# Kernel tuning notes

Measured on AMD Instinct MI355X. Metric: run time of the kernel, lower is better.

The kernel has to match this reference:

```python
import jax, jax.numpy as jnp
import numpy as np

N = 50000
E = 800000
HID = 128
OUT = 64
HEADS = 4
NEG_SLOPE = 0.2


def gat_layer(x, edge_index, W, att_src, att_dst, bias):
    """PyG-style GATConv: shared linear for src/dst, additive attention,
    self-loops, segment softmax over incoming edges, concat heads + bias."""
    n = x.shape[0]
    H, C = att_src.shape
    # add self loops (PyG default add_self_loops=True)
    loops = jnp.arange(n, dtype=edge_index.dtype)
    src = jnp.concatenate([edge_index[0], loops])  # message sources j
    dst = jnp.concatenate([edge_index[1], loops])  # aggregation targets i
    xl = (x @ W).reshape(n, H, C)                  # [N,H,C]
    a_s = jnp.einsum('nhc,hc->nh', xl, att_src)    # [N,H]
    a_d = jnp.einsum('nhc,hc->nh', xl, att_dst)    # [N,H]
    e = jax.nn.leaky_relu(a_s[src] + a_d[dst], NEG_SLOPE)   # [E',H]
    m = jax.ops.segment_max(e, dst, num_segments=n)         # stable softmax
    e = jnp.exp(e - m[dst])
    denom = jax.ops.segment_sum(e, dst, num_segments=n)
    alpha = e / (denom[dst] + 1e-16)                        # [E',H]
    msg = xl[src] * alpha[:, :, None]                       # [E',H,C]
    out = jax.ops.segment_sum(msg, dst, num_segments=n)     # [N,H,C]
    return out.reshape(n, H * C) + bias


def setup_inputs() -> dict:
    key = jax.random.key(0)
    ks = jax.random.split(key, 16)
    C = HID // HEADS  # per-head channels = 32
    x = jax.random.normal(ks[0], (N, HID), dtype=jnp.float32)
    edge_indices = jax.random.randint(ks[1], (3, 2, E), 0, N, dtype=jnp.int32)
    s = 0.1
    inp = {
        'x': x,
        'edge_indices': edge_indices,
        'W1': jax.random.normal(ks[2], (HID, HEADS * C), dtype=jnp.float32) * s,
        'as1': jax.random.normal(ks[3], (HEADS, C), dtype=jnp.float32) * s,
        'ad1': jax.random.normal(ks[4], (HEADS, C), dtype=jnp.float32) * s,
        'b1': jnp.zeros((HEADS * C,), dtype=jnp.float32),
        'W2': jax.random.normal(ks[5], (HID, HEADS * C), dtype=jnp.float32) * s,
        'as2': jax.random.normal(ks[6], (HEADS, C), dtype=jnp.float32) * s,
        'ad2': jax.random.normal(ks[7], (HEADS, C), dtype=jnp.float32) * s,
        'b2': jnp.zeros((HEADS * C,), dtype=jnp.float32),
        'W3': jax.random.normal(ks[8], (HID, OUT), dtype=jnp.float32) * s,
        'as3': jax.random.normal(ks[9], (1, OUT), dtype=jnp.float32) * s,
        'ad3': jax.random.normal(ks[10], (1, OUT), dtype=jnp.float32) * s,
        'b3': jnp.zeros((OUT,), dtype=jnp.float32),
    }
    return inp


def reference(x, edge_indices, W1, as1, ad1, b1, W2, as2, ad2, b2, W3, as3, ad3, b3):
    h = jax.nn.relu(gat_layer(x, edge_indices[0], W1, as1, ad1, b1))
    h = jax.nn.relu(gat_layer(h, edge_indices[1], W2, as2, ad2, b2))
    out = gat_layer(h, edge_indices[2], W3, as3, ad3, b3)  # no ReLU on last layer
    return out
```

## Files before the change

kernel.cpp:

```cpp
#include <hip/hip_runtime.h>

typedef unsigned short u16;
typedef unsigned int u32;
typedef __attribute__((ext_vector_type(8))) short short8;
typedef __attribute__((ext_vector_type(4))) float f32x4;

#define HID 128

static inline int cdiv(long long a, int b) { return (int)((a + b - 1) / b); }

__device__ __forceinline__ float bfbits(u32 u) { union { u32 u; float f; } c; c.u = u; return c.f; }
__device__ __forceinline__ u16 f2bf(float f) {
  union { float f; u32 u; } c; c.f = f;
  u32 u = c.u;
  return (u16)((u + 0x7fffu + ((u >> 16) & 1u)) >> 16);
}
__device__ __forceinline__ u32 pack2bf(float a, float b) {
  return (u32)f2bf(a) | ((u32)f2bf(b) << 16);
}

__global__ __launch_bounds__(256) void prep_wt3(
    const float* __restrict__ W1, const float* __restrict__ W2,
    const float* __restrict__ W3, u16* __restrict__ wt1, u16* __restrict__ wt2,
    u16* __restrict__ wt3) {
  int y = blockIdx.y;
  const float* W = (y == 0) ? W1 : ((y == 1) ? W2 : W3);
  u16* WT = (y == 0) ? wt1 : ((y == 1) ? wt2 : wt3);
  int cout = (y == 2) ? 64 : 128;
  int idx = blockIdx.x * 256 + threadIdx.x;
  if (idx < 128 * cout) {
    int k = idx / cout, c = idx - k * cout;
    WT[c * 128 + k] = f2bf(W[idx]);
  }
}

template <int COUT, int HEADS, bool BF16IN>
__global__ __launch_bounds__(256) void gemm_attn_mfma(
    const void* __restrict__ HinV, const u16* __restrict__ WT,
    const float* __restrict__ attS, const float* __restrict__ attD,
    u16* __restrict__ XL, float* __restrict__ aS, float* __restrict__ aD, int n) {
  constexpr int NT = COUT / 16;
  constexpr int C = COUT / HEADS;
  constexpr int TPH = C / 16;

  int t = threadIdx.x;
  int wv = t >> 6, ln = t & 63;
  int lrow = ln & 15;
  int lk = ln >> 4;
  int row = blockIdx.x * 64 + wv * 16 + lrow;
  bool ok = (row < n);
  int rowc = ok ? row : (n - 1);

  short8 bb[4];
  if (BF16IN) {
    const u16* hp = (const u16*)HinV + (size_t)rowc * HID;
#pragma unroll
    for (int kb = 0; kb < 4; ++kb)
      bb[kb] = *(const short8*)(hp + kb * 32 + lk * 8);
  } else {
    const float* hp = (const float*)HinV + (size_t)rowc * HID;
    float4 hv[8];
#pragma unroll
    for (int kb = 0; kb < 4; ++kb) {
      hv[2 * kb] = *(const float4*)(hp + kb * 32 + lk * 8);
      hv[2 * kb + 1] = *(const float4*)(hp + kb * 32 + lk * 8 + 4);
    }
#pragma unroll
    for (int kb = 0; kb < 4; ++kb) {
      union { short8 s; u32 u[4]; } pk;
      float4 h0 = hv[2 * kb], h1 = hv[2 * kb + 1];
      pk.u[0] = pack2bf(h0.x, h0.y);
      pk.u[1] = pack2bf(h0.z, h0.w);
      pk.u[2] = pack2bf(h1.x, h1.y);
      pk.u[3] = pack2bf(h1.z, h1.w);
      bb[kb] = pk.s;
    }
  }

  f32x4 acc[NT];
#pragma unroll
  for (int ct = 0; ct < NT; ++ct) acc[ct] = {0.f, 0.f, 0.f, 0.f};

#pragma unroll
  for (int kb = 0; kb < 4; ++kb) {
    const u16* wp = WT + (size_t)lrow * HID + kb * 32 + lk * 8;
#pragma unroll
    for (int ct = 0; ct < NT; ++ct) {
      short8 aw = *(const short8*)(wp + (size_t)ct * 16 * HID);
      acc[ct] = __builtin_amdgcn_mfma_f32_16x16x32_bf16(aw, bb[kb], acc[ct], 0, 0, 0);
    }
  }

  float pS[HEADS], pD[HEADS];
#pragma unroll
  for (int h = 0; h < HEADS; ++h) { pS[h] = 0.f; pD[h] = 0.f; }
#pragma unroll
  for (int ct = 0; ct < NT; ++ct) {
    float4 sv = *(const float4*)(attS + ct * 16 + lk * 4);
    float4 dv = *(const float4*)(attD + ct * 16 + lk * 4);
    int h = ct / TPH;
    pS[h] += acc[ct][0] * sv.x + acc[ct][1] * sv.y + acc[ct][2] * sv.z + acc[ct][3] * sv.w;
    pD[h] += acc[ct][0] * dv.x + acc[ct][1] * dv.y + acc[ct][2] * dv.z + acc[ct][3] * dv.w;
  }
#pragma unroll
  for (int h = 0; h < HEADS; ++h) {
    pS[h] += __shfl_xor(pS[h], 16);
    pS[h] += __shfl_xor(pS[h], 32);
    pD[h] += __shfl_xor(pD[h], 16);
    pD[h] += __shfl_xor(pD[h], 32);
  }
  if (lk == 0 && ok) {
    if (HEADS == 4) {
      *(float4*)(aS + (size_t)row * 4) = make_float4(pS[0], pS[1], pS[2], pS[3]);
      *(float4*)(aD + (size_t)row * 4) = make_float4(pD[0], pD[1], pD[2], pD[3]);
    } else {
      aS[row] = pS[0];
      aD[row] = pD[0];
    }
  }

  if (ok) {
    u32* Xp = (u32*)XL + (size_t)row * (COUT / 2);
#pragma unroll
    for (int ct = 0; ct < NT; ++ct) {
      *(uint2*)(Xp + ct * 8 + lk * 2) =
          make_uint2(pack2bf(acc[ct][0], acc[ct][1]), pack2bf(acc[ct][2], acc[ct][3]));
    }
  }
}

#define PSTR 16

__global__ __launch_bounds__(256) void bucket_hist(const int* __restrict__ ei,
                                                   int* __restrict__ cntP,
                                                   int e4, int rem, int E, int NB) {
  int L = blockIdx.y;
  const int* dst = ei + (size_t)(2 * L + 1) * E;
  __shared__ int cnt[256];
  int t = threadIdx.x;
  cnt[t] = 0;
  __syncthreads();
  int gbase = blockIdx.x * 1024 + t;
#pragma unroll
  for (int u = 0; u < 4; ++u) {
    int g = gbase + u * 256;
    if (g < e4) {
      int4 d = *(const int4*)(dst + g * 4);
      atomicAdd(&cnt[d.x >> 8], 1);
      atomicAdd(&cnt[d.y >> 8], 1);
      atomicAdd(&cnt[d.z >> 8], 1);
      atomicAdd(&cnt[d.w >> 8], 1);
    }
  }
  if (blockIdx.x == 0 && t < rem) atomicAdd(&cnt[dst[e4 * 4 + t] >> 8], 1);
  __syncthreads();
  int c = cnt[t];
  if (t < NB && c > 0) atomicAdd(&cntP[(L * NB + t) * PSTR], c);
}

__global__ __launch_bounds__(256) void bucket_scan(const int* __restrict__ cntP,
                                                   int* __restrict__ bucketOff,
                                                   int* __restrict__ curP, int NB, int E) {
  int L = blockIdx.x;
  int t = threadIdx.x;
  int lane = t & 63, wid = t >> 6;
  __shared__ int wpart[4];
  int v = (t < NB) ? cntP[(L * NB + t) * PSTR] : 0;
  int inc = v;
#pragma unroll
  for (int off = 1; off < 64; off <<= 1) {
    int w = __shfl_up(inc, (unsigned)off, 64);
    if (lane >= off) inc += w;
  }
  if (lane == 63) wpart[wid] = inc;
  __syncthreads();
  if (t == 0) {
    int a = 0;
#pragma unroll
    for (int k = 0; k < 4; ++k) { int tmp = wpart[k]; wpart[k] = a; a += tmp; }
  }
  __syncthreads();
  int ex = wpart[wid] + inc - v;
  if (t < NB) {
    bucketOff[L * (NB + 1) + t] = ex;
    curP[(L * NB + t) * PSTR] = ex;
  }
  if (t == 0) bucketOff[L * (NB + 1) + NB] = E;
}

__global__ __launch_bounds__(256) void bucket_scatter(const int* __restrict__ ei,
                                                      int* __restrict__ curP,
                                                      u32* __restrict__ pairsAll,
                                                      int e4, int rem, int E, int NB) {
  int L = blockIdx.y;
  const int* src = ei + (size_t)(2 * L) * E;
  const int* dst = src + E;
  u32* pairs = pairsAll + (size_t)L * E;
  __shared__ int cnt[256];
  __shared__ int baseS[256];
  int t = threadIdx.x;
  cnt[t] = 0;
  __syncthreads();

  int gbase = blockIdx.x * 1024 + t;
  int4 dv[4], sv[4];
  bool val[4];
#pragma unroll
  for (int u = 0; u < 4; ++u) {
    int g = gbase + u * 256;
    val[u] = (g < e4);
    if (val[u]) {
      dv[u] = *(const int4*)(dst + g * 4);
      sv[u] = *(const int4*)(src + g * 4);
      atomicAdd(&cnt[dv[u].x >> 8], 1);
      atomicAdd(&cnt[dv[u].y >> 8], 1);
      atomicAdd(&cnt[dv[u].z >> 8], 1);
      atomicAdd(&cnt[dv[u].w >> 8], 1);
    }
  }
  int tailS = 0, tailD = 0;
  bool hasTail = (blockIdx.x == 0 && t < rem);
  if (hasTail) {
    tailD = dst[e4 * 4 + t];
    tailS = src[e4 * 4 + t];
    atomicAdd(&cnt[tailD >> 8], 1);
  }
  __syncthreads();
  int c = cnt[t];
  if (t < NB && c > 0) baseS[t] = atomicAdd(&curP[(L * NB + t) * PSTR], c);
  __syncthreads();
  cnt[t] = 0;
  __syncthreads();
#pragma unroll
  for (int u = 0; u < 4; ++u) {
    if (val[u]) {
      int b, p;
      b = dv[u].x >> 8; p = atomicAdd(&cnt[b], 1);
      pairs[baseS[b] + p] = ((u32)(dv[u].x & 0xff) << 24) | (u32)sv[u].x;
      b = dv[u].y >> 8; p = atomicAdd(&cnt[b], 1);
      pairs[baseS[b] + p] = ((u32)(dv[u].y & 0xff) << 24) | (u32)sv[u].y;
      b = dv[u].z >> 8; p = atomicAdd(&cnt[b], 1);
      pairs[baseS[b] + p] = ((u32)(dv[u].z & 0xff) << 24) | (u32)sv[u].z;
      b = dv[u].w >> 8; p = atomicAdd(&cnt[b], 1);
      pairs[baseS[b] + p] = ((u32)(dv[u].w & 0xff) << 24) | (u32)sv[u].w;
    }
  }
  if (hasTail) {
    int b = tailD >> 8;
    int p = atomicAdd(&cnt[b], 1);
    pairs[baseS[b] + p] = ((u32)(tailD & 0xff) << 24) | (u32)tailS;
  }
}

__global__ __launch_bounds__(256) void csr_finalize(const u32* __restrict__ pairsAll,
                                                    const int* __restrict__ bucketOff,
                                                    int* __restrict__ indptrAll,
                                                    int* __restrict__ srcIdxAll,
                                                    int* __restrict__ dstIdxAll,
                                                    int N, int E, int NB) {
  int L = blockIdx.y, b = blockIdx.x;
  const u32* pairs = pairsAll + (size_t)L * E;
  int* indptr = indptrAll + (size_t)L * (N + 1);
  int* srcL = srcIdxAll + (size_t)L * (E + N);
  int* dstL = dstIdxAll + (size_t)L * (E + N);
  int base = b << 8;
  int nodes = min(256, N - base);
  int p0 = bucketOff[L * (NB + 1) + b];
  int p1 = bucketOff[L * (NB + 1) + b + 1];

  __shared__ int cnt[256];
  __shared__ int wpart[4];
  int t = threadIdx.x;
  int lane = t & 63, wid = t >> 6;
  cnt[t] = 0;
  __syncthreads();

  for (int i = p0 + t; i < p1; i += 256) atomicAdd(&cnt[pairs[i] >> 24], 1);
  __syncthreads();

  int v = (t < nodes) ? cnt[t] + 1 : 0;
  int inc = v;
#pragma unroll
  for (int off = 1; off < 64; off <<= 1) {
    int w = __shfl_up(inc, (unsigned)off, 64);
    if (lane >= off) inc += w;
  }
  if (lane == 63) wpart[wid] = inc;
  __syncthreads();
  if (t == 0) {
    int a = 0;
#pragma unroll
    for (int k = 0; k < 4; ++k) { int tmp = wpart[k]; wpart[k] = a; a += tmp; }
  }
  __syncthreads();
  int ex = wpart[wid] + inc - v;
  __syncthreads();
  if (t < nodes) {
    int segStart = p0 + base + ex;
    indptr[base + t] = segStart;
    srcL[segStart] = base + t;
    dstL[segStart] = base + t;
    cnt[t] = segStart + 1;
  }
  if (b == NB - 1 && t == 0) indptr[N] = E + N;
  __syncthreads();

  for (int i = p0 + t; i < p1; i += 256) {
    u32 pk = pairs[i];
    int d = (int)(pk >> 24);
    int p = atomicAdd(&cnt[d], 1);
    srcL[p] = (int)(pk & 0xffffffu);
    dstL[p] = base + d;
  }
}

template <int HEADS>
__global__ __launch_bounds__(256) void edge_w_ep(
    const float* __restrict__ aS, const float* __restrict__ aD,
    const int* __restrict__ srcL, const int* __restrict__ dstL,
    float* __restrict__ wOut, int ne, int wstride) {
  int e = blockIdx.x * 256 + threadIdx.x;
  if (e >= ne) return;
  int j = srcL[e];
  int i = dstL[e];
  if (HEADS == 4) {
    float4 s4 = *(const float4*)(aS + (size_t)j * 4);
    float4 d4 = *(const float4*)(aD + (size_t)i * 4);
    float l0 = s4.x + d4.x, l1 = s4.y + d4.y, l2 = s4.z + d4.z, l3 = s4.w + d4.w;
    l0 = (l0 >= 0.f) ? l0 : 0.2f * l0;
    l1 = (l1 >= 0.f) ? l1 : 0.2f * l1;
    l2 = (l2 >= 0.f) ? l2 : 0.2f * l2;
    l3 = (l3 >= 0.f) ? l3 : 0.2f * l3;
    wOut[e] = __expf(fminf(l0, 60.f));
    wOut[(size_t)wstride + e] = __expf(fminf(l1, 60.f));
    wOut[(size_t)2 * wstride + e] = __expf(fminf(l2, 60.f));
    wOut[(size_t)3 * wstride + e] = __expf(fminf(l3, 60.f));
  } else {
    float l = aS[j] + aD[i];
    l = (l >= 0.f) ? l : 0.2f * l;
    wOut[e] = __expf(fminf(l, 60.f));
  }
}

template <int COUT, int HEADS, bool RELU, bool OUTBF>
__global__ __launch_bounds__(256, 8) void aggregate(
    const u16* __restrict__ XL, const float* __restrict__ wAll,
    const int* __restrict__ indptr, const int* __restrict__ srcIdx,
    const float* __restrict__ bias, void* __restrict__ outV, int n, int wstride) {
  constexpr int LPN = COUT / 8;
  constexpr int NPW = 64 / LPN;
  constexpr int C = COUT / HEADS;

  int wid = (blockIdx.x * blockDim.x + threadIdx.x) >> 6;
  int lane = threadIdx.x & 63;
  int sub = lane / LPN;
  int cl = lane % LPN;
  int i = wid * NPW + sub;
  bool ok = (i < n);
  int ic = ok ? i : (n - 1);

  int col0 = cl * 8;
  int h = col0 / C;
  int e0 = indptr[ic];
  int deg = indptr[ic + 1] - e0;
  const float* wh = wAll + (size_t)h * wstride;
  const u32* XL32 = (const u32*)XL;

  float s = 0.f;
  float acc[8];
#pragma unroll
  for (int v = 0; v < 8; ++v) acc[v] = 0.f;

  auto cons = [&](float el, const uint4& q) {
    s += el;
    acc[0] += el * bfbits(q.x << 16);
    acc[1] += el * bfbits(q.x & 0xffff0000u);
    acc[2] += el * bfbits(q.y << 16);
    acc[3] += el * bfbits(q.y & 0xffff0000u);
    acc[4] += el * bfbits(q.z << 16);
    acc[5] += el * bfbits(q.z & 0xffff0000u);
    acc[6] += el * bfbits(q.w << 16);
    acc[7] += el * bfbits(q.w & 0xffff0000u);
  };
  auto xlrow = [&](int j) {
    return *(const uint4*)(XL32 + (size_t)j * (COUT / 2) + cl * 4);
  };

  int nbF = deg >> 2;
  int r = deg & 3;

  int4 jA;
  float4 wA;
  if (nbF > 0) {
    jA = *(const int4*)(srcIdx + e0);
    wA = *(const float4*)(wh + e0);
  }
  for (int b = 0; b < nbF; ++b) {
    int4 jC = jA;
    float4 wC = wA;
    if (b + 1 < nbF) {
      jA = *(const int4*)(srcIdx + e0 + (b + 1) * 4);
      wA = *(const float4*)(wh + e0 + (b + 1) * 4);
    }
    uint4 q0 = xlrow(jC.x);
    uint4 q1 = xlrow(jC.y);
    uint4 q2 = xlrow(jC.z);
    uint4 q3 = xlrow(jC.w);
    cons(wC.x, q0);
    cons(wC.y, q1);
    cons(wC.z, q2);
    cons(wC.w, q3);
  }
  if (r) {
    int e = e0 + nbF * 4;
    int j0 = srcIdx[e];
    int j1 = (r > 1) ? srcIdx[e + 1] : 0;
    int j2 = (r > 2) ? srcIdx[e + 2] : 0;
    float w0 = wh[e];
    float w1 = (r > 1) ? wh[e + 1] : 0.f;
    float w2 = (r > 2) ? wh[e + 2] : 0.f;
    uint4 q0 = xlrow(j0);
    uint4 q1 = xlrow(j1);
    uint4 q2 = xlrow(j2);
    cons(w0, q0);
    if (r > 1) cons(w1, q1);
    if (r > 2) cons(w2, q2);
  }

  if (!ok) return;
  float inv = 1.f / (s + 1e-16f);
  float o[8];
#pragma unroll
  for (int v = 0; v < 8; ++v) {
    o[v] = acc[v] * inv + bias[col0 + v];
    if (RELU) o[v] = fmaxf(o[v], 0.f);
  }
  if (OUTBF) {
    u32* op = (u32*)outV + (size_t)i * (COUT / 2) + cl * 4;
    *(uint4*)op = make_uint4(pack2bf(o[0], o[1]), pack2bf(o[2], o[3]),
                             pack2bf(o[4], o[5]), pack2bf(o[6], o[7]));
  } else {
    float* op = (float*)outV + (size_t)i * COUT + col0;
    *(float4*)op = make_float4(o[0], o[1], o[2], o[3]);
    *(float4*)(op + 4) = make_float4(o[4], o[5], o[6], o[7]);
  }
}

extern "C" void kernel_launch(void* const* d_in, const int* in_sizes, int n_in,
                              void* d_out, int out_size, void* d_ws, size_t ws_size,
                              hipStream_t stream) {
  const float* x = (const float*)d_in[0];
  const int* ei = (const int*)d_in[1];
  const float* W1 = (const float*)d_in[2];
  const float* as1 = (const float*)d_in[3];
  const float* ad1 = (const float*)d_in[4];
  const float* b1 = (const float*)d_in[5];
  const float* W2 = (const float*)d_in[6];
  const float* as2 = (const float*)d_in[7];
  const float* ad2 = (const float*)d_in[8];
  const float* b2 = (const float*)d_in[9];
  const float* W3 = (const float*)d_in[10];
  const float* as3 = (const float*)d_in[11];
  const float* ad3 = (const float*)d_in[12];
  const float* b3 = (const float*)d_in[13];

  int N = in_sizes[0] / HID;
  int E = in_sizes[1] / 6;
  int NB = cdiv(N, 256);
  int EN = E + N;

  char* w = (char*)d_ws;
  auto alloc = [&](size_t bytes) {
    void* q = (void*)w;
    w += (bytes + 255) & ~(size_t)255;
    return q;
  };
  u16* bufH = (u16*)alloc((size_t)N * HID * 2);
  u16* bufXL = (u16*)alloc((size_t)N * HID * 2);
  float* aS = (float*)alloc((size_t)N * 4 * 4);
  float* aD = (float*)alloc((size_t)N * 4 * 4);
  float* wEdge = (float*)alloc((size_t)4 * EN * 4);
  u16* wt1 = (u16*)alloc((size_t)128 * 128 * 2);
  u16* wt2 = (u16*)alloc((size_t)128 * 128 * 2);
  u16* wt3 = (u16*)alloc((size_t)64 * 128 * 2);
  int* cntP = (int*)alloc((size_t)3 * NB * PSTR * 4);
  int* curP = (int*)alloc((size_t)3 * NB * PSTR * 4);
  int* bucketOff = (int*)alloc((size_t)3 * (NB + 1) * 4);
  u32* pairsAll = (u32*)alloc((size_t)3 * E * 4);
  int* indptrAll = (int*)alloc((size_t)3 * (N + 1) * 4);
  int* srcIdxAll = (int*)alloc((size_t)3 * EN * 4);
  int* dstIdxAll = (int*)alloc((size_t)3 * EN * 4);

  int e4 = E >> 2, rem = E & 3;
  int gx = cdiv(e4, 1024);
  int gne = cdiv(EN, 256);

  {
    dim3 g(64, 3);
    prep_wt3<<<g, 256, 0, stream>>>(W1, W2, W3, wt1, wt2, wt3);
  }
  hipMemsetAsync(cntP, 0, (size_t)3 * NB * PSTR * 4, stream);
  {
    dim3 g(gx, 3);
    bucket_hist<<<g, 256, 0, stream>>>(ei, cntP, e4, rem, E, NB);
  }
  bucket_scan<<<3, 256, 0, stream>>>(cntP, bucketOff, curP, NB, E);
  {
    dim3 g(gx, 3);
    bucket_scatter<<<g, 256, 0, stream>>>(ei, curP, pairsAll, e4, rem, E, NB);
  }
  {
    dim3 g(NB, 3);
    csr_finalize<<<g, 256, 0, stream>>>(pairsAll, bucketOff, indptrAll, srcIdxAll,
                                        dstIdxAll, N, E, NB);
  }

  gemm_attn_mfma<128, 4, false><<<cdiv(N, 64), 256, 0, stream>>>(
      x, wt1, as1, ad1, bufXL, aS, aD, N);
  edge_w_ep<4><<<gne, 256, 0, stream>>>(aS, aD, srcIdxAll, dstIdxAll, wEdge, EN, EN);
  aggregate<128, 4, true, true><<<cdiv(N, 16), 256, 0, stream>>>(
      bufXL, wEdge, indptrAll, srcIdxAll, b1, bufH, N, EN);
  gemm_attn_mfma<128, 4, true><<<cdiv(N, 64), 256, 0, stream>>>(
      bufH, wt2, as2, ad2, bufXL, aS, aD, N);
  edge_w_ep<4><<<gne, 256, 0, stream>>>(aS, aD, srcIdxAll + (size_t)EN,
                                        dstIdxAll + (size_t)EN, wEdge, EN, EN);
  aggregate<128, 4, true, true><<<cdiv(N, 16), 256, 0, stream>>>(
      bufXL, wEdge, indptrAll + (N + 1), srcIdxAll + (size_t)EN, b2, bufH, N, EN);
  gemm_attn_mfma<64, 1, true><<<cdiv(N, 64), 256, 0, stream>>>(
      bufH, wt3, as3, ad3, bufXL, aS, aD, N);
  edge_w_ep<1><<<gne, 256, 0, stream>>>(aS, aD, srcIdxAll + (size_t)2 * EN,
                                        dstIdxAll + (size_t)2 * EN, wEdge, EN, EN);
  aggregate<64, 1, false, false><<<cdiv(N, 32), 256, 0, stream>>>(
      bufXL, wEdge, indptrAll + 2 * (N + 1), srcIdxAll + (size_t)2 * EN, b3,
      d_out, N, EN);
}
```

Measured before the change: 361.1 us.

## Fold weight prep and layer-1 GEMM into CSR build kernels; stage finalize in LDS

Weight transpose/convert runs as an extra grid row inside the bucket histogram kernel. The layer-1 projection GEMM runs as an extra grid row inside the bucket scatter kernel, so it overlaps with CSR construction and two launches disappear. csr_finalize now builds each bucket's segment in shared memory and writes it out contiguously, falling back to direct global writes when the bucket is too large. The 64 KB of LDS per block can lower finalize occupancy, and the fused kernels mix unrelated work, which may change their register pressure.

```diff
diff --git a/kernel.cpp b/kernel.cpp
--- a/kernel.cpp
+++ b/kernel.cpp
@@ -19,35 +19,19 @@
   return (u32)f2bf(a) | ((u32)f2bf(b) << 16);
 }
 
-__global__ __launch_bounds__(256) void prep_wt3(
-    const float* __restrict__ W1, const float* __restrict__ W2,
-    const float* __restrict__ W3, u16* __restrict__ wt1, u16* __restrict__ wt2,
-    u16* __restrict__ wt3) {
-  int y = blockIdx.y;
-  const float* W = (y == 0) ? W1 : ((y == 1) ? W2 : W3);
-  u16* WT = (y == 0) ? wt1 : ((y == 1) ? wt2 : wt3);
-  int cout = (y == 2) ? 64 : 128;
-  int idx = blockIdx.x * 256 + threadIdx.x;
-  if (idx < 128 * cout) {
-    int k = idx / cout, c = idx - k * cout;
-    WT[c * 128 + k] = f2bf(W[idx]);
-  }
-}
-
 template <int COUT, int HEADS, bool BF16IN>
-__global__ __launch_bounds__(256) void gemm_attn_mfma(
-    const void* __restrict__ HinV, const u16* __restrict__ WT,
+__device__ __forceinline__ void gemm_body(
+    int bx, int t, const void* __restrict__ HinV, const u16* __restrict__ WT,
     const float* __restrict__ attS, const float* __restrict__ attD,
     u16* __restrict__ XL, float* __restrict__ aS, float* __restrict__ aD, int n) {
   constexpr int NT = COUT / 16;
   constexpr int C = COUT / HEADS;
   constexpr int TPH = C / 16;
 
-  int t = threadIdx.x;
   int wv = t >> 6, ln = t & 63;
   int lrow = ln & 15;
   int lk = ln >> 4;
-  int row = blockIdx.x * 64 + wv * 16 + lrow;
+  int row = bx * 64 + wv * 16 + lrow;
   bool ok = (row < n);
   int rowc = ok ? row : (n - 1);
 
@@ -129,11 +113,37 @@
   }
 }
 
+template <int COUT, int HEADS, bool BF16IN>
+__global__ __launch_bounds__(256) void gemm_attn_mfma(
+    const void* __restrict__ HinV, const u16* __restrict__ WT,
+    const float* __restrict__ attS, const float* __restrict__ attD,
+    u16* __restrict__ XL, float* __restrict__ aS, float* __restrict__ aD, int n) {
+  gemm_body<COUT, HEADS, BF16IN>(blockIdx.x, threadIdx.x, HinV, WT, attS, attD,
+                                 XL, aS, aD, n);
+}
+
 #define PSTR 16
 
-__global__ __launch_bounds__(256) void bucket_hist(const int* __restrict__ ei,
-                                                   int* __restrict__ cntP,
-                                                   int e4, int rem, int E, int NB) {
+__global__ __launch_bounds__(256) void bucket_hist_prep(
+    const int* __restrict__ ei, int* __restrict__ cntP, int e4, int rem, int E, int NB,
+    const float* __restrict__ W1, const float* __restrict__ W2,
+    const float* __restrict__ W3, u16* __restrict__ wt1, u16* __restrict__ wt2,
+    u16* __restrict__ wt3) {
+  if (blockIdx.y == 3) {
+    int bx = blockIdx.x;
+    if (bx >= 160) return;
+    int y = (bx >= 128) ? 2 : (bx >= 64 ? 1 : 0);
+    int b0 = (y == 0) ? 0 : ((y == 1) ? 64 : 128);
+    const float* W = (y == 0) ? W1 : ((y == 1) ? W2 : W3);
+    u16* WT = (y == 0) ? wt1 : ((y == 1) ? wt2 : wt3);
+    int cout = (y == 2) ? 64 : 128;
+    int idx = (bx - b0) * 256 + threadIdx.x;
+    if (idx < 128 * cout) {
+      int k = idx / cout, c = idx - k * cout;
+      WT[c * 128 + k] = f2bf(W[idx]);
+    }
+    return;
+  }
   int L = blockIdx.y;
   const int* dst = ei + (size_t)(2 * L + 1) * E;
   __shared__ int cnt[256];
@@ -188,10 +198,18 @@
   if (t == 0) bucketOff[L * (NB + 1) + NB] = E;
 }
 
-__global__ __launch_bounds__(256) void bucket_scatter(const int* __restrict__ ei,
-                                                      int* __restrict__ curP,
-                                                      u32* __restrict__ pairsAll,
-                                                      int e4, int rem, int E, int NB) {
+__global__ __launch_bounds__(256) void bucket_scatter_gemm(
+    const int* __restrict__ ei, int* __restrict__ curP, u32* __restrict__ pairsAll,
+    int e4, int rem, int E, int NB,
+    const float* __restrict__ x, const u16* __restrict__ wt1,
+    const float* __restrict__ as1, const float* __restrict__ ad1,
+    u16* __restrict__ XL, float* __restrict__ aS, float* __restrict__ aD,
+    int n, int ngb) {
+  if (blockIdx.y == 3) {
+    if ((int)blockIdx.x < ngb)
+      gemm_body<128, 4, false>(blockIdx.x, threadIdx.x, x, wt1, as1, ad1, XL, aS, aD, n);
+    return;
+  }
   int L = blockIdx.y;
   const int* src = ei + (size_t)(2 * L) * E;
   const int* dst = src + E;
@@ -252,6 +270,7 @@
   }
 }
 
+#define FCAP 8192
 __global__ __launch_bounds__(256) void csr_finalize(const u32* __restrict__ pairsAll,
                                                     const int* __restrict__ bucketOff,
                                                     int* __restrict__ indptrAll,
@@ -270,6 +289,8 @@
 
   __shared__ int cnt[256];
   __shared__ int wpart[4];
+  __shared__ int sSrc[FCAP];
+  __shared__ int sDst[FCAP];
   int t = threadIdx.x;
   int lane = t & 63, wid = t >> 6;
   cnt[t] = 0;
@@ -294,23 +315,45 @@
   }
   __syncthreads();
   int ex = wpart[wid] + inc - v;
+  int tot = (p1 - p0) + nodes;
+  bool useLds = (tot <= FCAP);
+  int g0 = p0 + base;
   __syncthreads();
   if (t < nodes) {
-    int segStart = p0 + base + ex;
-    indptr[base + t] = segStart;
-    srcL[segStart] = base + t;
-    dstL[segStart] = base + t;
-    cnt[t] = segStart + 1;
+    indptr[base + t] = g0 + ex;
+    if (useLds) {
+      sSrc[ex] = base + t;
+      sDst[ex] = base + t;
+    } else {
+      srcL[g0 + ex] = base + t;
+      dstL[g0 + ex] = base + t;
+    }
+    cnt[t] = ex + 1;
   }
   if (b == NB - 1 && t == 0) indptr[N] = E + N;
   __syncthreads();
 
-  for (int i = p0 + t; i < p1; i += 256) {
-    u32 pk = pairs[i];
-    int d = (int)(pk >> 24);
-    int p = atomicAdd(&cnt[d], 1);
-    srcL[p] = (int)(pk & 0xffffffu);
-    dstL[p] = base + d;
+  if (useLds) {
+    for (int i = p0 + t; i < p1; i += 256) {
+      u32 pk = pairs[i];
+      int d = (int)(pk >> 24);
+      int p = atomicAdd(&cnt[d], 1);
+      sSrc[p] = (int)(pk & 0xffffffu);
+      sDst[p] = base + d;
+    }
+    __syncthreads();
+    for (int k = t; k < tot; k += 256) {
+      srcL[g0 + k] = sSrc[k];
+      dstL[g0 + k] = sDst[k];
+    }
+  } else {
+    for (int i = p0 + t; i < p1; i += 256) {
+      u32 pk = pairs[i];
+      int d = (int)(pk >> 24);
+      int p = atomicAdd(&cnt[d], 1);
+      srcL[g0 + p] = (int)(pk & 0xffffffu);
+      dstL[g0 + p] = base + d;
+    }
   }
 }
 
@@ -493,21 +536,22 @@
 
   int e4 = E >> 2, rem = E & 3;
   int gx = cdiv(e4, 1024);
+  int ngb = cdiv(N, 64);
   int gne = cdiv(EN, 256);
-
-  {
-    dim3 g(64, 3);
-    prep_wt3<<<g, 256, 0, stream>>>(W1, W2, W3, wt1, wt2, wt3);
-  }
+  int gxh = (gx > 160) ? gx : 160;
+  int gxs = (gx > ngb) ? gx : ngb;
+
   hipMemsetAsync(cntP, 0, (size_t)3 * NB * PSTR * 4, stream);
   {
-    dim3 g(gx, 3);
-    bucket_hist<<<g, 256, 0, stream>>>(ei, cntP, e4, rem, E, NB);
+    dim3 g(gxh, 4);
+    bucket_hist_prep<<<g, 256, 0, stream>>>(ei, cntP, e4, rem, E, NB,
+                                            W1, W2, W3, wt1, wt2, wt3);
   }
   bucket_scan<<<3, 256, 0, stream>>>(cntP, bucketOff, curP, NB, E);
   {
-    dim3 g(gx, 3);
-    bucket_scatter<<<g, 256, 0, stream>>>(ei, curP, pairsAll, e4, rem, E, NB);
+    dim3 g(gxs, 4);
+    bucket_scatter_gemm<<<g, 256, 0, stream>>>(ei, curP, pairsAll, e4, rem, E, NB,
+                                               x, wt1, as1, ad1, bufXL, aS, aD, N, ngb);
   }
   {
     dim3 g(NB, 3);
@@ -515,8 +559,6 @@
                                         dstIdxAll, N, E, NB);
   }
 
-  gemm_attn_mfma<128, 4, false><<<cdiv(N, 64), 256, 0, stream>>>(
-      x, wt1, as1, ad1, bufXL, aS, aD, N);
   edge_w_ep<4><<<gne, 256, 0, stream>>>(aS, aD, srcIdxAll, dstIdxAll, wEdge, EN, EN);
   aggregate<128, 4, true, true><<<cdiv(N, 16), 256, 0, stream>>>(
       bufXL, wEdge, indptrAll, srcIdxAll, b1, bufH, N, EN);
```

After: 327.5 us. 1.1x faster.
